# Kernel optimization log

Measured on AMD Instinct MI355X. Metric: run time of the kernel, lower is better.

## Reference

```python
import jax, jax.numpy as jnp
import numpy as np
from jax import lax

# Norse default LIF/LI parameters with dt=0.001
DT_TAU_MEM = 0.1   # dt * tau_mem_inv (1/1e-2)
DT_TAU_SYN = 0.2   # dt * tau_syn_inv (1/5e-3)
V_TH = 0.5
ALPHA = 100.0      # SuperSpike surrogate slope (backward only)

@jax.custom_vjp
def spike(x):
    return (x > 0).astype(x.dtype)

def _spike_fwd(x):
    return (x > 0).astype(x.dtype), x

def _spike_bwd(x, g):
    # SuperSpike surrogate gradient: 1 / (alpha*|x| + 1)^2
    sg = 1.0 / (ALPHA * jnp.abs(x) + 1.0) ** 2
    return (g * sg,)

spike.defvjp(_spike_fwd, _spike_bwd)

def setup_inputs() -> dict:
    key = jax.random.key(0)
    k1, k2, k3 = jax.random.split(key, 3)
    T, B, C, H, W = 64, 512, 1, 28, 28
    IN, HID, OUT = 784, 2048, 10
    x = jax.random.normal(k1, (T, B, C, H, W), dtype=jnp.float32)
    # Kaiming-uniform-ish bias-free Linear weights, torch layout [out, in]
    w1 = jax.random.uniform(k2, (HID, IN), jnp.float32, -1.0, 1.0) / np.sqrt(IN)
    w_out = jax.random.uniform(k3, (OUT, HID), jnp.float32, -1.0, 1.0) / np.sqrt(HID)
    return {"x": x, "w1": w1, "w_out": w_out}

def reference(x, w1, w_out):
    T, B = x.shape[0], x.shape[1]
    HID, OUT = w1.shape[0], w_out.shape[0]
    xf = x.reshape(T, B, -1)  # [T, B, IN]

    def step(carry, xt):
        v1, i1, vo, io = carry
        cur = xt @ w1.T                       # fc1: [B, HID]
        # LIF: decay, threshold/spike/reset, then integrate new input current
        v1_dec = v1 + DT_TAU_MEM * (-v1 + i1)
        i1_dec = i1 * (1.0 - DT_TAU_SYN)
        z = spike(v1_dec - V_TH)
        v1_new = (1.0 - z) * v1_dec           # v_reset = 0
        i1_new = i1_dec + cur
        out_cur = z @ w_out.T                 # fc_out: [B, OUT]
        # LI readout: leaky integration (no spiking)
        vo_new = vo + DT_TAU_MEM * (-vo + io)
        io_new = io * (1.0 - DT_TAU_SYN) + out_cur
        return (v1_new, i1_new, vo_new, io_new), vo_new

    zh = jnp.zeros((B, HID), x.dtype)
    zo = jnp.zeros((B, OUT), x.dtype)
    _, voltages = lax.scan(step, (zh, zh, zo, zo), xf)  # [T, B, OUT]
    return jnp.max(voltages, axis=0)
```

## Files before the change

### kernel.cpp

```cpp
#include <hip/hip_runtime.h>
#include <cstdint>
#include <cstddef>

#define T_STEPS 64
#define BATCH 512
#define IN_F 784
#define NKT 25
#define HID 2048
#define OUT_F 10

#define DEC_V 0.9f
#define DEC_I 0.8f
#define DT_V 0.1f
#define V_TH 0.5f

typedef __attribute__((ext_vector_type(8))) _Float16 f16x8;
typedef __attribute__((ext_vector_type(4))) float f32x4;

__device__ __forceinline__ void load_lds16h(const _Float16* g, _Float16* l) {
  __builtin_amdgcn_global_load_lds(
      (const __attribute__((address_space(1))) void*)g,
      (__attribute__((address_space(3))) void*)l, 16, 0, 0);
}

#define VMCNT(N)                                                     \
  do {                                                               \
    asm volatile("s_waitcnt vmcnt(" #N ")" ::: "memory");            \
    __builtin_amdgcn_sched_barrier(0);                               \
  } while (0)
#define LGKM0                                                        \
  do {                                                               \
    asm volatile("s_waitcnt lgkmcnt(0)" ::: "memory");               \
    __builtin_amdgcn_sched_barrier(0);                               \
  } while (0)

__global__ __launch_bounds__(256)
void split_frag(const float* __restrict__ src, _Float16* __restrict__ hiT,
                _Float16* __restrict__ loT) {
  __shared__ float xr[16][804];
  const int mt = blockIdx.x;
  for (int i = threadIdx.x; i < 16 * IN_F; i += 256) {
    const int r = i / IN_F, c = i - r * IN_F;
    xr[r][c] = src[(size_t)(mt * 16 + r) * IN_F + c];
  }
  for (int i = threadIdx.x; i < 16 * 16; i += 256)
    xr[i >> 4][IN_F + (i & 15)] = 0.0f;
  __syncthreads();

  const int l = threadIdx.x & 63;
  const int g = threadIdx.x >> 6;
  const int r = l & 15, q = l >> 4;
  for (int kt = g; kt < NKT; kt += 4) {
    const float* s = &xr[r][kt * 32 + q * 8];
    f16x8 h, lo;
#pragma unroll
    for (int j = 0; j < 8; ++j) {
      const float v = s[j];
      const _Float16 hh = (_Float16)v;
      h[j] = hh;
      lo[j] = (_Float16)(v - (float)hh);
    }
    const size_t off = ((size_t)mt * NKT + kt) * 512 + l * 8;
    *(f16x8*)&hiT[off] = h;
    *(f16x8*)&loT[off] = lo;
  }
}

__global__ __launch_bounds__(512, 2)
void gemm_fc1(const _Float16* __restrict__ AhT, const _Float16* __restrict__ AlT,
              const _Float16* __restrict__ WhT, const _Float16* __restrict__ WlT,
              float* __restrict__ C) {
  __shared__ _Float16 __attribute__((aligned(16))) sAh[2][16 * 512];
  __shared__ _Float16 __attribute__((aligned(16))) sAl[2][16 * 512];
  __shared__ _Float16 __attribute__((aligned(16))) sWh[2][16 * 512];
  __shared__ _Float16 __attribute__((aligned(16))) sWl[2][16 * 512];

  const int tid = threadIdx.x;
  const int lane = tid & 63;
  const int wv = tid >> 6;

  const int nwg = gridDim.x * gridDim.y;
  const int bid = blockIdx.y * gridDim.x + blockIdx.x;
  const int q = nwg >> 3;
  const int swz = (bid & 7) * q + (bid >> 3);
  const int bx = swz & 7;
  const int by = swz >> 3;

  const int bmT = by * 16;
  const int bnT = bx * 16;

  const int wr = wv >> 2;
  const int wc = wv & 3;
  const int col = lane & 15;
  const int quad = lane >> 4;

  f32x4 acc[8][4] = {};

#define STAGE(KT, BUF)                                                       \
  do {                                                                       \
    _Pragma("unroll")                                                        \
    for (int j = 0; j < 2; ++j) {                                            \
      const int t = wv * 2 + j;                                              \
      const size_t ga = ((size_t)(bmT + t) * NKT + (KT)) * 512 + lane * 8;   \
      load_lds16h(AhT + ga, &sAh[BUF][t * 512]);                             \
      load_lds16h(AlT + ga, &sAl[BUF][t * 512]);                             \
      const size_t gw = ((size_t)(bnT + t) * NKT + (KT)) * 512 + lane * 8;   \
      load_lds16h(WhT + gw, &sWh[BUF][t * 512]);                             \
      load_lds16h(WlT + gw, &sWl[BUF][t * 512]);                             \
    }                                                                        \
  } while (0)

  STAGE(0, 0);

  for (int kt = 0; kt < NKT; ++kt) {
    const int cur = kt & 1;
    if (kt + 1 < NKT) {
      STAGE(kt + 1, cur ^ 1);
      VMCNT(8);
    } else {
      VMCNT(0);
    }
    __builtin_amdgcn_s_barrier();

    f16x8 fah[8], fal[8];
#pragma unroll
    for (int i = 0; i < 8; ++i) {
      fah[i] = *(const f16x8*)&sAh[cur][(wr * 8 + i) * 512 + lane * 8];
      fal[i] = *(const f16x8*)&sAl[cur][(wr * 8 + i) * 512 + lane * 8];
    }
#pragma unroll
    for (int nj = 0; nj < 4; ++nj) {
      const f16x8 fwh = *(const f16x8*)&sWh[cur][(wc * 4 + nj) * 512 + lane * 8];
      const f16x8 fwl = *(const f16x8*)&sWl[cur][(wc * 4 + nj) * 512 + lane * 8];
#pragma unroll
      for (int mi = 0; mi < 8; ++mi) {
        acc[mi][nj] = __builtin_amdgcn_mfma_f32_16x16x32_f16(fah[mi], fwh, acc[mi][nj], 0, 0, 0);
        acc[mi][nj] = __builtin_amdgcn_mfma_f32_16x16x32_f16(fah[mi], fwl, acc[mi][nj], 0, 0, 0);
        acc[mi][nj] = __builtin_amdgcn_mfma_f32_16x16x32_f16(fal[mi], fwh, acc[mi][nj], 0, 0, 0);
      }
    }
    LGKM0;
    __builtin_amdgcn_s_barrier();
  }
#undef STAGE

  const int rowb = by * 256 + wr * 128;
  const int colb = bx * 256 + wc * 64;
#pragma unroll
  for (int mi = 0; mi < 8; ++mi)
#pragma unroll
    for (int r = 0; r < 4; ++r) {
      const size_t rowo = (size_t)(rowb + mi * 16 + quad * 4 + r) * HID;
#pragma unroll
      for (int nj = 0; nj < 4; ++nj)
        C[rowo + colb + nj * 16 + col] = acc[mi][nj][r];
    }
}

__global__ __launch_bounds__(256)
void lif_out(const float* __restrict__ cur, const float* __restrict__ wo,
             float* __restrict__ v1, float* __restrict__ i1,
             float* __restrict__ outP, int tc, int t0) {
  __shared__ _Float16 zL[T_STEPS][264];
  __shared__ _Float16 wT[16][264];

  const int tid = threadIdx.x;
  const int hc = blockIdx.x;
  const int b = blockIdx.y;
  const int hb = hc * 256;

  for (int i = tid; i < 16 * 256; i += 256) {
    const int n = i >> 8, k = i & 255;
    wT[n][k] = (n < OUT_F) ? (_Float16)wo[(size_t)n * HID + hb + k] : (_Float16)0.f;
  }

  const int sidx = b * HID + hb + tid;
  float v = v1[sidx];
  float ci = i1[sidx];
#pragma unroll 4
  for (int t = 0; t < tc; ++t) {
    const float c = cur[(size_t)t * (BATCH * HID) + sidx];
    const float vd = DEC_V * v + DT_V * ci;
    const float z = (vd > V_TH) ? 1.0f : 0.0f;
    v = (1.0f - z) * vd;
    ci = DEC_I * ci + c;
    zL[t][tid] = (_Float16)z;
  }
  v1[sidx] = v;
  i1[sidx] = ci;
  __syncthreads();

  const int wv = tid >> 6;
  const int lane = tid & 63;
  const int col = lane & 15;
  const int quad = lane >> 4;
  f32x4 acc = {};
  const _Float16* za = &zL[wv * 16 + col][0];
  const _Float16* wb = &wT[col][0];
#pragma unroll
  for (int ks = 0; ks < 8; ++ks) {
    f16x8 a = *(const f16x8*)(za + ks * 32 + quad * 8);
    f16x8 bb = *(const f16x8*)(wb + ks * 32 + quad * 8);
    acc = __builtin_amdgcn_mfma_f32_16x16x32_f16(a, bb, acc, 0, 0, 0);
  }
  if (col < OUT_F) {
#pragma unroll
    for (int r = 0; r < 4; ++r) {
      const int t = wv * 16 + quad * 4 + r;
      if (t < tc)
        outP[(((size_t)hc * T_STEPS + (t0 + t)) * BATCH + b) * OUT_F + col] = acc[r];
    }
  }
}

__global__ __launch_bounds__(256)
void li_scan(const float* __restrict__ outP, float* __restrict__ out) {
  const int idx = blockIdx.x * 256 + threadIdx.x;
  if (idx >= BATCH * OUT_F) return;
  float vo = 0.f, io = 0.f, vmax = 0.f;
  for (int t = 0; t < T_STEPS; ++t) {
    float oc = 0.f;
#pragma unroll
    for (int hc = 0; hc < 8; ++hc)
      oc += outP[((size_t)hc * T_STEPS + t) * (BATCH * OUT_F) + idx];
    const float von = DEC_V * vo + DT_V * io;
    io = DEC_I * io + oc;
    vo = von;
    vmax = fmaxf(vmax, von);
  }
  out[idx] = vmax;
}

__global__ void zero_state(float* __restrict__ p, int n) {
  int i = blockIdx.x * 256 + threadIdx.x;
  if (i < n) p[i] = 0.0f;
}

extern "C" void kernel_launch(void* const* d_in, const int* in_sizes, int n_in,
                              void* d_out, int out_size, void* d_ws, size_t ws_size,
                              hipStream_t stream) {
  const float* x  = (const float*)d_in[0];
  const float* w1 = (const float*)d_in[1];
  const float* wo = (const float*)d_in[2];
  float* out = (float*)d_out;

  const size_t BH = (size_t)BATCH * HID;
  const size_t WT_HALVES = (size_t)(HID / 16) * NKT * 512;

  float* v1 = (float*)d_ws;
  float* i1 = v1 + BH;
  float* outP = i1 + BH;
  _Float16* WhT = (_Float16*)(outP + (size_t)8 * T_STEPS * BATCH * OUT_F);
  _Float16* WlT = WhT + WT_HALVES;
  char* chunk0 = (char*)(WlT + WT_HALVES);

  const size_t base_bytes = (size_t)(chunk0 - (char*)d_ws);
  const size_t per_step = BH * 4 + (size_t)2 * 32 * NKT * 512 * 2;
  int Tc = T_STEPS;
  while (Tc > 1 && base_bytes + (size_t)Tc * per_step > ws_size) Tc >>= 1;

  float* cur = (float*)chunk0;
  _Float16* AhT = (_Float16*)(cur + (size_t)Tc * BH);
  _Float16* AlT = AhT + (size_t)Tc * 32 * NKT * 512;

  split_frag<<<HID / 16, 256, 0, stream>>>(w1, WhT, WlT);
  zero_state<<<(int)((2 * BH + 255) / 256), 256, 0, stream>>>(v1, (int)(2 * BH));

  for (int t0 = 0; t0 < T_STEPS; t0 += Tc) {
    const int tc = (T_STEPS - t0 < Tc) ? (T_STEPS - t0) : Tc;
    const int nrows = tc * BATCH;
    split_frag<<<nrows / 16, 256, 0, stream>>>(x + (size_t)t0 * BATCH * IN_F, AhT, AlT);
    dim3 grid(HID / 256, nrows / 256);
    gemm_fc1<<<grid, 512, 0, stream>>>(AhT, AlT, WhT, WlT, cur);
    dim3 lgrid(HID / 256, BATCH);
    lif_out<<<lgrid, 256, 0, stream>>>(cur, wo, v1, i1, outP, tc, t0);
  }
  li_scan<<<(BATCH * OUT_F + 255) / 256, 256, 0, stream>>>(outP, out);
}
```

Measured before the change: 614.9 us.

## Interleave LDS fragment loads, prefetch and MFMA phases in the fc1 GEMM loop

The split-fp16 GEMM main loop is rebuilt as four sub-phases, each covering half of the M and N fragments. Global-to-LDS prefetch of the next k-tile is split into A and W halves and issued between phases, and each MFMA block runs under raised wave priority via s_setprio. The goal is to overlap LDS reads, global prefetch and MFMA work and to lower register pressure from fragments, instead of loading everything and then computing. The cost is more barriers per k-tile and a wait for all outstanding loads at the end of every iteration.

```diff
diff --git a/kernel.cpp b/kernel.cpp
--- a/kernel.cpp
+++ b/kernel.cpp
@@ -23,9 +23,9 @@
       (__attribute__((address_space(3))) void*)l, 16, 0, 0);
 }
 
-#define VMCNT(N)                                                     \
+#define VMCNT0                                                       \
   do {                                                               \
-    asm volatile("s_waitcnt vmcnt(" #N ")" ::: "memory");            \
+    asm volatile("s_waitcnt vmcnt(0)" ::: "memory");                 \
     __builtin_amdgcn_sched_barrier(0);                               \
   } while (0)
 #define LGKM0                                                        \
@@ -33,6 +33,9 @@
     asm volatile("s_waitcnt lgkmcnt(0)" ::: "memory");               \
     __builtin_amdgcn_sched_barrier(0);                               \
   } while (0)
+#define BAR __builtin_amdgcn_s_barrier()
+#define PRIO1 __builtin_amdgcn_s_setprio(1)
+#define PRIO0 __builtin_amdgcn_s_setprio(0)
 
 __global__ __launch_bounds__(256)
 void split_frag(const float* __restrict__ src, _Float16* __restrict__ hiT,
@@ -95,8 +98,10 @@
   const int quad = lane >> 4;
 
   f32x4 acc[8][4] = {};
-
-#define STAGE(KT, BUF)                                                       \
+  f16x8 fah[4], fal[4];
+  f16x8 fwh[4], fwl[4];
+
+#define STAGE_A(KT, BUF)                                                     \
   do {                                                                       \
     _Pragma("unroll")                                                        \
     for (int j = 0; j < 2; ++j) {                                            \
@@ -104,45 +109,91 @@
       const size_t ga = ((size_t)(bmT + t) * NKT + (KT)) * 512 + lane * 8;   \
       load_lds16h(AhT + ga, &sAh[BUF][t * 512]);                             \
       load_lds16h(AlT + ga, &sAl[BUF][t * 512]);                             \
+    }                                                                        \
+  } while (0)
+
+#define STAGE_W(KT, BUF)                                                     \
+  do {                                                                       \
+    _Pragma("unroll")                                                        \
+    for (int j = 0; j < 2; ++j) {                                            \
+      const int t = wv * 2 + j;                                              \
       const size_t gw = ((size_t)(bnT + t) * NKT + (KT)) * 512 + lane * 8;   \
       load_lds16h(WhT + gw, &sWh[BUF][t * 512]);                             \
       load_lds16h(WlT + gw, &sWl[BUF][t * 512]);                             \
     }                                                                        \
   } while (0)
 
-  STAGE(0, 0);
+#define DS_A(MH)                                                             \
+  do {                                                                       \
+    _Pragma("unroll")                                                        \
+    for (int i = 0; i < 4; ++i) {                                            \
+      fah[i] = *(const f16x8*)&sAh[cur][(wr * 8 + (MH) * 4 + i) * 512 + lane * 8]; \
+      fal[i] = *(const f16x8*)&sAl[cur][(wr * 8 + (MH) * 4 + i) * 512 + lane * 8]; \
+    }                                                                        \
+  } while (0)
+
+#define DS_W(NH)                                                             \
+  do {                                                                       \
+    _Pragma("unroll")                                                        \
+    for (int j = 0; j < 2; ++j) {                                            \
+      fwh[(NH) * 2 + j] = *(const f16x8*)&sWh[cur][(wc * 4 + (NH) * 2 + j) * 512 + lane * 8]; \
+      fwl[(NH) * 2 + j] = *(const f16x8*)&sWl[cur][(wc * 4 + (NH) * 2 + j) * 512 + lane * 8]; \
+    }                                                                        \
+  } while (0)
+
+#define MM(MH, NH)                                                           \
+  do {                                                                       \
+    _Pragma("unroll")                                                        \
+    for (int j = 0; j < 2; ++j)                                              \
+      _Pragma("unroll")                                                      \
+      for (int i = 0; i < 4; ++i) {                                          \
+        acc[(MH) * 4 + i][(NH) * 2 + j] = __builtin_amdgcn_mfma_f32_16x16x32_f16( \
+            fah[i], fwh[(NH) * 2 + j], acc[(MH) * 4 + i][(NH) * 2 + j], 0, 0, 0); \
+        acc[(MH) * 4 + i][(NH) * 2 + j] = __builtin_amdgcn_mfma_f32_16x16x32_f16( \
+            fah[i], fwl[(NH) * 2 + j], acc[(MH) * 4 + i][(NH) * 2 + j], 0, 0, 0); \
+        acc[(MH) * 4 + i][(NH) * 2 + j] = __builtin_amdgcn_mfma_f32_16x16x32_f16( \
+            fal[i], fwh[(NH) * 2 + j], acc[(MH) * 4 + i][(NH) * 2 + j], 0, 0, 0); \
+      }                                                                      \
+  } while (0)
+
+  STAGE_A(0, 0);
+  STAGE_W(0, 0);
+  VMCNT0;
+  BAR;
 
   for (int kt = 0; kt < NKT; ++kt) {
     const int cur = kt & 1;
-    if (kt + 1 < NKT) {
-      STAGE(kt + 1, cur ^ 1);
-      VMCNT(8);
-    } else {
-      VMCNT(0);
-    }
-    __builtin_amdgcn_s_barrier();
-
-    f16x8 fah[8], fal[8];
-#pragma unroll
-    for (int i = 0; i < 8; ++i) {
-      fah[i] = *(const f16x8*)&sAh[cur][(wr * 8 + i) * 512 + lane * 8];
-      fal[i] = *(const f16x8*)&sAl[cur][(wr * 8 + i) * 512 + lane * 8];
-    }
-#pragma unroll
-    for (int nj = 0; nj < 4; ++nj) {
-      const f16x8 fwh = *(const f16x8*)&sWh[cur][(wc * 4 + nj) * 512 + lane * 8];
-      const f16x8 fwl = *(const f16x8*)&sWl[cur][(wc * 4 + nj) * 512 + lane * 8];
-#pragma unroll
-      for (int mi = 0; mi < 8; ++mi) {
-        acc[mi][nj] = __builtin_amdgcn_mfma_f32_16x16x32_f16(fah[mi], fwh, acc[mi][nj], 0, 0, 0);
-        acc[mi][nj] = __builtin_amdgcn_mfma_f32_16x16x32_f16(fah[mi], fwl, acc[mi][nj], 0, 0, 0);
-        acc[mi][nj] = __builtin_amdgcn_mfma_f32_16x16x32_f16(fal[mi], fwh, acc[mi][nj], 0, 0, 0);
-      }
-    }
+    const bool pf = (kt + 1 < NKT);
+
+    DS_A(0);
+    DS_W(0);
+    if (pf) STAGE_A(kt + 1, cur ^ 1);
+    BAR;
     LGKM0;
-    __builtin_amdgcn_s_barrier();
-  }
-#undef STAGE
+    PRIO1; MM(0, 0); PRIO0;
+    BAR;
+
+    DS_W(1);
+    if (pf) STAGE_W(kt + 1, cur ^ 1);
+    BAR;
+    LGKM0;
+    PRIO1; MM(0, 1); PRIO0;
+    BAR;
+
+    DS_A(1);
+    BAR;
+    LGKM0;
+    PRIO1; MM(1, 0);
+    VMCNT0;
+    PRIO0;
+    BAR;
+    PRIO1; MM(1, 1); PRIO0;
+  }
+#undef STAGE_A
+#undef STAGE_W
+#undef DS_A
+#undef DS_W
+#undef MM
 
   const int rowb = by * 256 + wr * 128;
   const int colb = bx * 256 + wc * 64;
```

Measured after the change: 597.5 us. -2.8%, faster.

## Shrink fc1 GEMM tile to 128x256 with triple-buffered LDS and MFMA priority

Applied to the files above, without the earlier changes.

The fc1 GEMM block tile is halved in M from 256 to 128 rows, which doubles the grid. The LDS pipeline goes from double to triple buffering, with two stages prefetched ahead and the vmcnt waits adjusted to match. Waves raise their priority with s_setprio around the MFMA loop, and the XCD-aware block swizzle is dropped. The aim is better latency hiding and more workgroups in flight, at the cost of lower arithmetic intensity per block, more loads of the weight tile, and losing the swizzle's L2 locality.

```diff
diff --git a/kernel.cpp b/kernel.cpp
--- a/kernel.cpp
+++ b/kernel.cpp
@@ -33,6 +33,9 @@
     asm volatile("s_waitcnt lgkmcnt(0)" ::: "memory");               \
     __builtin_amdgcn_sched_barrier(0);                               \
   } while (0)
+#define BAR __builtin_amdgcn_s_barrier()
+#define PRIO1 __builtin_amdgcn_s_setprio(1)
+#define PRIO0 __builtin_amdgcn_s_setprio(0)
 
 __global__ __launch_bounds__(256)
 void split_frag(const float* __restrict__ src, _Float16* __restrict__ hiT,
@@ -70,84 +73,86 @@
 void gemm_fc1(const _Float16* __restrict__ AhT, const _Float16* __restrict__ AlT,
               const _Float16* __restrict__ WhT, const _Float16* __restrict__ WlT,
               float* __restrict__ C) {
-  __shared__ _Float16 __attribute__((aligned(16))) sAh[2][16 * 512];
-  __shared__ _Float16 __attribute__((aligned(16))) sAl[2][16 * 512];
-  __shared__ _Float16 __attribute__((aligned(16))) sWh[2][16 * 512];
-  __shared__ _Float16 __attribute__((aligned(16))) sWl[2][16 * 512];
+  __shared__ _Float16 __attribute__((aligned(16))) sAh[3][8 * 512];
+  __shared__ _Float16 __attribute__((aligned(16))) sAl[3][8 * 512];
+  __shared__ _Float16 __attribute__((aligned(16))) sWh[3][16 * 512];
+  __shared__ _Float16 __attribute__((aligned(16))) sWl[3][16 * 512];
 
   const int tid = threadIdx.x;
   const int lane = tid & 63;
   const int wv = tid >> 6;
 
-  const int nwg = gridDim.x * gridDim.y;
-  const int bid = blockIdx.y * gridDim.x + blockIdx.x;
-  const int q = nwg >> 3;
-  const int swz = (bid & 7) * q + (bid >> 3);
-  const int bx = swz & 7;
-  const int by = swz >> 3;
-
-  const int bmT = by * 16;
-  const int bnT = bx * 16;
+  const int bmT = blockIdx.y * 8;
+  const int bnT = blockIdx.x * 16;
 
   const int wr = wv >> 2;
   const int wc = wv & 3;
   const int col = lane & 15;
   const int quad = lane >> 4;
 
-  f32x4 acc[8][4] = {};
-
-#define STAGE(KT, BUF)                                                       \
+  f32x4 acc[4][4] = {};
+
+#define STAGE(KT, B)                                                         \
   do {                                                                       \
+    const size_t ga = ((size_t)(bmT + wv) * NKT + (KT)) * 512 + lane * 8;    \
+    load_lds16h(AhT + ga, &sAh[B][wv * 512]);                                \
+    load_lds16h(AlT + ga, &sAl[B][wv * 512]);                                \
     _Pragma("unroll")                                                        \
     for (int j = 0; j < 2; ++j) {                                            \
       const int t = wv * 2 + j;                                              \
-      const size_t ga = ((size_t)(bmT + t) * NKT + (KT)) * 512 + lane * 8;   \
-      load_lds16h(AhT + ga, &sAh[BUF][t * 512]);                             \
-      load_lds16h(AlT + ga, &sAl[BUF][t * 512]);                             \
       const size_t gw = ((size_t)(bnT + t) * NKT + (KT)) * 512 + lane * 8;   \
-      load_lds16h(WhT + gw, &sWh[BUF][t * 512]);                             \
-      load_lds16h(WlT + gw, &sWl[BUF][t * 512]);                             \
+      load_lds16h(WhT + gw, &sWh[B][t * 512]);                               \
+      load_lds16h(WlT + gw, &sWl[B][t * 512]);                               \
     }                                                                        \
   } while (0)
 
   STAGE(0, 0);
-
+  STAGE(1, 1);
+
+  int b0 = 0;
+  int bs = 2;
   for (int kt = 0; kt < NKT; ++kt) {
-    const int cur = kt & 1;
-    if (kt + 1 < NKT) {
-      STAGE(kt + 1, cur ^ 1);
-      VMCNT(8);
+    if (kt + 2 < NKT) {
+      STAGE(kt + 2, bs);
+      VMCNT(12);
+    } else if (kt + 2 == NKT) {
+      VMCNT(6);
     } else {
       VMCNT(0);
     }
-    __builtin_amdgcn_s_barrier();
-
-    f16x8 fah[8], fal[8];
-#pragma unroll
-    for (int i = 0; i < 8; ++i) {
-      fah[i] = *(const f16x8*)&sAh[cur][(wr * 8 + i) * 512 + lane * 8];
-      fal[i] = *(const f16x8*)&sAl[cur][(wr * 8 + i) * 512 + lane * 8];
-    }
+    BAR;
+    __builtin_amdgcn_sched_barrier(0);
+
+    f16x8 fah[4], fal[4];
+#pragma unroll
+    for (int i = 0; i < 4; ++i) {
+      fah[i] = *(const f16x8*)&sAh[b0][(wr * 4 + i) * 512 + lane * 8];
+      fal[i] = *(const f16x8*)&sAl[b0][(wr * 4 + i) * 512 + lane * 8];
+    }
+    PRIO1;
 #pragma unroll
     for (int nj = 0; nj < 4; ++nj) {
-      const f16x8 fwh = *(const f16x8*)&sWh[cur][(wc * 4 + nj) * 512 + lane * 8];
-      const f16x8 fwl = *(const f16x8*)&sWl[cur][(wc * 4 + nj) * 512 + lane * 8];
-#pragma unroll
-      for (int mi = 0; mi < 8; ++mi) {
+      const f16x8 fwh = *(const f16x8*)&sWh[b0][(wc * 4 + nj) * 512 + lane * 8];
+      const f16x8 fwl = *(const f16x8*)&sWl[b0][(wc * 4 + nj) * 512 + lane * 8];
+#pragma unroll
+      for (int mi = 0; mi < 4; ++mi) {
         acc[mi][nj] = __builtin_amdgcn_mfma_f32_16x16x32_f16(fah[mi], fwh, acc[mi][nj], 0, 0, 0);
         acc[mi][nj] = __builtin_amdgcn_mfma_f32_16x16x32_f16(fah[mi], fwl, acc[mi][nj], 0, 0, 0);
         acc[mi][nj] = __builtin_amdgcn_mfma_f32_16x16x32_f16(fal[mi], fwh, acc[mi][nj], 0, 0, 0);
       }
     }
+    PRIO0;
     LGKM0;
-    __builtin_amdgcn_s_barrier();
+    BAR;
+    b0 = (b0 == 2) ? 0 : b0 + 1;
+    bs = (bs == 2) ? 0 : bs + 1;
   }
 #undef STAGE
 
-  const int rowb = by * 256 + wr * 128;
-  const int colb = bx * 256 + wc * 64;
-#pragma unroll
-  for (int mi = 0; mi < 8; ++mi)
+  const int rowb = blockIdx.y * 128 + wr * 64;
+  const int colb = blockIdx.x * 256 + wc * 64;
+#pragma unroll
+  for (int mi = 0; mi < 4; ++mi)
 #pragma unroll
     for (int r = 0; r < 4; ++r) {
       const size_t rowo = (size_t)(rowb + mi * 16 + quad * 4 + r) * HID;
@@ -270,7 +275,7 @@
     const int tc = (T_STEPS - t0 < Tc) ? (T_STEPS - t0) : Tc;
     const int nrows = tc * BATCH;
     split_frag<<<nrows / 16, 256, 0, stream>>>(x + (size_t)t0 * BATCH * IN_F, AhT, AlT);
-    dim3 grid(HID / 256, nrows / 256);
+    dim3 grid(HID / 256, nrows / 128);
     gemm_fc1<<<grid, 512, 0, stream>>>(AhT, AlT, WhT, WlT, cur);
     dim3 lgrid(HID / 256, BATCH);
     lif_out<<<lgrid, 256, 0, stream>>>(cur, wo, v1, i1, outP, tc, t0);
```

Measured after the change: 678.4 us. 1.1x slower.
